# Kernel tuning notes

Measured on AMD Instinct MI355X. Metric: run time of the kernel, lower is better.

## Reference

```python
import jax, jax.numpy as jnp
import numpy as np

KERNEL_SIZE = 5
GROUP_SIZE = 1
SCALE = 2


def setup_inputs() -> dict:
    key = jax.random.key(0)
    k1, k2 = jax.random.split(key)
    N, C, H, W = 2, 256, 128, 128
    features = jax.random.normal(k1, (N, C, H, W), dtype=jnp.float32)
    masks = jax.random.uniform(
        k2, (N, KERNEL_SIZE * KERNEL_SIZE * GROUP_SIZE, H * SCALE, W * SCALE),
        dtype=jnp.float32)
    return {"features": features, "masks": masks}


def reference(features, masks):
    # CARAFE: content-aware reassembly upsampling.
    # out[n,c,i,j] = sum_{dy,dx} feat[n,c, i//s + dy - r, j//s + dx - r]
    #                * masks[n, g*K*K + dy*K + dx, i, j]
    K, G, s = KERNEL_SIZE, GROUP_SIZE, SCALE
    N, C, H, W = features.shape
    Cg = C // G
    K2 = K * K
    r = K // 2
    # zero-pad spatially and gather all K*K shifted views -> (N, C, K2, H, W)
    fp = jnp.pad(features, ((0, 0), (0, 0), (r, r), (r, r)))
    patches = jnp.stack(
        [fp[:, :, dy:dy + H, dx:dx + W] for dy in range(K) for dx in range(K)],
        axis=2)
    patches = patches.reshape(N, G, Cg, K2, H, W)
    # masks at output resolution; split each output pixel into (src_pixel, subpixel)
    m = masks.reshape(N, G, K2, H, s, W, s)
    # weighted reduce over the kernel window, broadcast over channels in group
    out = jnp.einsum('ngckhw,ngkhawb->ngchawb', patches, m)
    return out.reshape(N, C, H * s, W * s)
```

## Files before the change

### kernel.cpp

```cpp
#include <hip/hip_runtime.h>

#define KK 5
#define RR 2
#define N_ 2
#define C_ 256
#define H_ 128
#define W_ 128
#define H2 256
#define W2 256
#define TW 32
#define TH 8
#define CCHUNK 8
#define PHh 12
#define PWw 36
#define NPIX (PHh*PWw)
#define PLANE (NPIX*4)
#define HW (H_*W_)
#define HW2 (H2*W2)
#define DEPTH 4

__global__ __launch_bounds__(256) void carafe_kernel(
    const float* __restrict__ feat,
    const float* __restrict__ masks,
    float* __restrict__ out)
{
    __shared__ float patch[2 * PLANE];

    const int tid = threadIdx.x;
    const int tx = tid & 31;
    const int ty = tid >> 5;

    const int bid   = blockIdx.x;
    const int xcd   = bid & 7;
    const int s     = bid >> 3;
    const int chunk = s & 31;
    const int tn    = xcd * 16 + (s >> 5);
    const int tile  = tn & 63;
    const int n     = tn >> 6;
    const int bx    = tile & 3;
    const int by    = tile >> 2;
    const int c0    = chunk * CCHUNK;

    const int i0 = by * TH + ty;
    const int j0 = bx * TW + tx;
    const int gy0 = by * TH - RR;
    const int gx0 = bx * TW - RR;

    const float* fbase = feat + (size_t)(n * C_ + c0) * HW;
    #pragma unroll
    for (int r = 0; r < 4; ++r) {
        const int idx = tid + r * 256;
        if (idx < 2 * NPIX) {
            const int G  = idx >= NPIX;
            const int p  = idx - G * NPIX;
            const int py = p / PWw;
            const int px = p - py * PWw;
            const int gy = gy0 + py;
            const int gx = gx0 + px;
            float4 v = make_float4(0.f, 0.f, 0.f, 0.f);
            if ((unsigned)gy < (unsigned)H_ && (unsigned)gx < (unsigned)W_) {
                const float* fp = fbase + (4 * G) * HW + gy * W_ + gx;
                v.x = fp[0];
                v.y = fp[HW];
                v.z = fp[2 * HW];
                v.w = fp[3 * HW];
            }
            *reinterpret_cast<float4*>(&patch[G * PLANE + p * 4]) = v;
        }
    }

    const float* mb = masks + ((size_t)n * (KK * KK) * H2 + (size_t)(2 * i0)) * W2 + 2 * j0;
    float2 q0[DEPTH], q1[DEPTH];
    #pragma unroll
    for (int t = 0; t < DEPTH; ++t) {
        q0[t] = *reinterpret_cast<const float2*>(mb + (size_t)t * HW2);
        q1[t] = *reinterpret_cast<const float2*>(mb + (size_t)t * HW2 + W2);
    }
    __syncthreads();

    float acc[CCHUNK][2][2] = {};
    const int p0 = ty * PWw + tx;

    #pragma unroll
    for (int k = 0; k < KK * KK; ++k) {
        const float2 m0 = q0[k % DEPTH];
        const float2 m1 = q1[k % DEPTH];
        if (k + DEPTH < KK * KK) {
            q0[k % DEPTH] = *reinterpret_cast<const float2*>(mb + (size_t)(k + DEPTH) * HW2);
            q1[k % DEPTH] = *reinterpret_cast<const float2*>(mb + (size_t)(k + DEPTH) * HW2 + W2);
        }
        const int dy = k / KK;
        const int dx = k - KK * dy;
        const int P  = p0 + dy * PWw + dx;
        const float4 v0 = *reinterpret_cast<const float4*>(&patch[P * 4]);
        const float4 v1 = *reinterpret_cast<const float4*>(&patch[PLANE + P * 4]);

        acc[0][0][0] += v0.x * m0.x;  acc[0][0][1] += v0.x * m0.y;
        acc[0][1][0] += v0.x * m1.x;  acc[0][1][1] += v0.x * m1.y;
        acc[1][0][0] += v0.y * m0.x;  acc[1][0][1] += v0.y * m0.y;
        acc[1][1][0] += v0.y * m1.x;  acc[1][1][1] += v0.y * m1.y;
        acc[2][0][0] += v0.z * m0.x;  acc[2][0][1] += v0.z * m0.y;
        acc[2][1][0] += v0.z * m1.x;  acc[2][1][1] += v0.z * m1.y;
        acc[3][0][0] += v0.w * m0.x;  acc[3][0][1] += v0.w * m0.y;
        acc[3][1][0] += v0.w * m1.x;  acc[3][1][1] += v0.w * m1.y;
        acc[4][0][0] += v1.x * m0.x;  acc[4][0][1] += v1.x * m0.y;
        acc[4][1][0] += v1.x * m1.x;  acc[4][1][1] += v1.x * m1.y;
        acc[5][0][0] += v1.y * m0.x;  acc[5][0][1] += v1.y * m0.y;
        acc[5][1][0] += v1.y * m1.x;  acc[5][1][1] += v1.y * m1.y;
        acc[6][0][0] += v1.z * m0.x;  acc[6][0][1] += v1.z * m0.y;
        acc[6][1][0] += v1.z * m1.x;  acc[6][1][1] += v1.z * m1.y;
        acc[7][0][0] += v1.w * m0.x;  acc[7][0][1] += v1.w * m0.y;
        acc[7][1][0] += v1.w * m1.x;  acc[7][1][1] += v1.w * m1.y;
    }

    float* ob = out + ((size_t)(n * C_ + c0) * H2 + (size_t)(2 * i0)) * W2 + 2 * j0;
    #pragma unroll
    for (int c = 0; c < CCHUNK; ++c) {
        *reinterpret_cast<float2*>(ob)      = make_float2(acc[c][0][0], acc[c][0][1]);
        *reinterpret_cast<float2*>(ob + W2) = make_float2(acc[c][1][0], acc[c][1][1]);
        ob += (size_t)HW2;
    }
}

extern "C" void kernel_launch(void* const* d_in, const int* in_sizes, int n_in,
                              void* d_out, int out_size, void* d_ws, size_t ws_size,
                              hipStream_t stream) {
    const float* feat  = (const float*)d_in[0];
    const float* masks = (const float*)d_in[1];
    float* out = (float*)d_out;

    carafe_kernel<<<dim3(4096), dim3(256), 0, stream>>>(feat, masks, out);
}
```

Measured before the change: 49.00 us.

## Remap threads to two pixels by four channels with register sliding window

Each thread now covers two adjacent source columns and four channels, not one column and eight channels. Per kernel row it loads six float4 patch values from LDS into registers and reuses them across the five dx taps, which cuts LDS reads. The LDS row stride is padded to avoid bank conflicts. Mask loads and output stores become 16-byte wide, and outputs use nontemporal stores. Mask values are now loaded twice, once by each channel-group half of the block.

```diff
diff --git a/kernel.cpp b/kernel.cpp
--- a/kernel.cpp
+++ b/kernel.cpp
@@ -13,11 +13,14 @@
 #define CCHUNK 8
 #define PHh 12
 #define PWw 36
+#define PWST 37
 #define NPIX (PHh*PWw)
-#define PLANE (NPIX*4)
+#define PLANE (PHh*PWST*4)
 #define HW (H_*W_)
 #define HW2 (H2*W2)
 #define DEPTH 4
+
+typedef float f32x4 __attribute__((ext_vector_type(4)));
 
 __global__ __launch_bounds__(256) void carafe_kernel(
     const float* __restrict__ feat,
@@ -27,8 +30,10 @@
     __shared__ float patch[2 * PLANE];
 
     const int tid = threadIdx.x;
-    const int tx = tid & 31;
-    const int ty = tid >> 5;
+    const int G   = tid >> 7;
+    const int pp  = tid & 127;
+    const int u   = pp & 15;
+    const int ty  = pp >> 4;
 
     const int bid   = blockIdx.x;
     const int xcd   = bid & 7;
@@ -42,7 +47,7 @@
     const int c0    = chunk * CCHUNK;
 
     const int i0 = by * TH + ty;
-    const int j0 = bx * TW + tx;
+    const int j0 = bx * TW + 2 * u;
     const int gy0 = by * TH - RR;
     const int gx0 = bx * TW - RR;
 
@@ -51,73 +56,72 @@
     for (int r = 0; r < 4; ++r) {
         const int idx = tid + r * 256;
         if (idx < 2 * NPIX) {
-            const int G  = idx >= NPIX;
-            const int p  = idx - G * NPIX;
+            const int Gs = idx >= NPIX;
+            const int p  = idx - Gs * NPIX;
             const int py = p / PWw;
             const int px = p - py * PWw;
             const int gy = gy0 + py;
             const int gx = gx0 + px;
             float4 v = make_float4(0.f, 0.f, 0.f, 0.f);
             if ((unsigned)gy < (unsigned)H_ && (unsigned)gx < (unsigned)W_) {
-                const float* fp = fbase + (4 * G) * HW + gy * W_ + gx;
+                const float* fp = fbase + (4 * Gs) * HW + gy * W_ + gx;
                 v.x = fp[0];
                 v.y = fp[HW];
                 v.z = fp[2 * HW];
                 v.w = fp[3 * HW];
             }
-            *reinterpret_cast<float4*>(&patch[G * PLANE + p * 4]) = v;
+            *reinterpret_cast<float4*>(&patch[Gs * PLANE + (py * PWST + px) * 4]) = v;
         }
     }
 
     const float* mb = masks + ((size_t)n * (KK * KK) * H2 + (size_t)(2 * i0)) * W2 + 2 * j0;
-    float2 q0[DEPTH], q1[DEPTH];
+    float4 q0[DEPTH], q1[DEPTH];
     #pragma unroll
     for (int t = 0; t < DEPTH; ++t) {
-        q0[t] = *reinterpret_cast<const float2*>(mb + (size_t)t * HW2);
-        q1[t] = *reinterpret_cast<const float2*>(mb + (size_t)t * HW2 + W2);
+        q0[t] = *reinterpret_cast<const float4*>(mb + (size_t)t * HW2);
+        q1[t] = *reinterpret_cast<const float4*>(mb + (size_t)t * HW2 + W2);
     }
     __syncthreads();
 
-    float acc[CCHUNK][2][2] = {};
-    const int p0 = ty * PWw + tx;
+    float acc[4][2][4] = {};
+    const int rbase = G * PLANE;
 
     #pragma unroll
-    for (int k = 0; k < KK * KK; ++k) {
-        const float2 m0 = q0[k % DEPTH];
-        const float2 m1 = q1[k % DEPTH];
-        if (k + DEPTH < KK * KK) {
-            q0[k % DEPTH] = *reinterpret_cast<const float2*>(mb + (size_t)(k + DEPTH) * HW2);
-            q1[k % DEPTH] = *reinterpret_cast<const float2*>(mb + (size_t)(k + DEPTH) * HW2 + W2);
+    for (int dy = 0; dy < KK; ++dy) {
+        const int row = ty + dy;
+        float4 w[6];
+        #pragma unroll
+        for (int j = 0; j < 6; ++j)
+            w[j] = *reinterpret_cast<const float4*>(&patch[rbase + (row * PWST + 2 * u + j) * 4]);
+
+        #pragma unroll
+        for (int dx = 0; dx < KK; ++dx) {
+            const int k = dy * KK + dx;
+            const float4 m0 = q0[k % DEPTH];
+            const float4 m1 = q1[k % DEPTH];
+            if (k + DEPTH < KK * KK) {
+                q0[k % DEPTH] = *reinterpret_cast<const float4*>(mb + (size_t)(k + DEPTH) * HW2);
+                q1[k % DEPTH] = *reinterpret_cast<const float4*>(mb + (size_t)(k + DEPTH) * HW2 + W2);
+            }
+            const float w0[4] = { w[dx].x,     w[dx].y,     w[dx].z,     w[dx].w     };
+            const float w1[4] = { w[dx + 1].x, w[dx + 1].y, w[dx + 1].z, w[dx + 1].w };
+            #pragma unroll
+            for (int t = 0; t < 4; ++t) {
+                acc[t][0][0] += w0[t] * m0.x;  acc[t][0][1] += w0[t] * m0.y;
+                acc[t][0][2] += w1[t] * m0.z;  acc[t][0][3] += w1[t] * m0.w;
+                acc[t][1][0] += w0[t] * m1.x;  acc[t][1][1] += w0[t] * m1.y;
+                acc[t][1][2] += w1[t] * m1.z;  acc[t][1][3] += w1[t] * m1.w;
+            }
         }
-        const int dy = k / KK;
-        const int dx = k - KK * dy;
-        const int P  = p0 + dy * PWw + dx;
-        const float4 v0 = *reinterpret_cast<const float4*>(&patch[P * 4]);
-        const float4 v1 = *reinterpret_cast<const float4*>(&patch[PLANE + P * 4]);
-
-        acc[0][0][0] += v0.x * m0.x;  acc[0][0][1] += v0.x * m0.y;
-        acc[0][1][0] += v0.x * m1.x;  acc[0][1][1] += v0.x * m1.y;
-        acc[1][0][0] += v0.y * m0.x;  acc[1][0][1] += v0.y * m0.y;
-        acc[1][1][0] += v0.y * m1.x;  acc[1][1][1] += v0.y * m1.y;
-        acc[2][0][0] += v0.z * m0.x;  acc[2][0][1] += v0.z * m0.y;
-        acc[2][1][0] += v0.z * m1.x;  acc[2][1][1] += v0.z * m1.y;
-        acc[3][0][0] += v0.w * m0.x;  acc[3][0][1] += v0.w * m0.y;
-        acc[3][1][0] += v0.w * m1.x;  acc[3][1][1] += v0.w * m1.y;
-        acc[4][0][0] += v1.x * m0.x;  acc[4][0][1] += v1.x * m0.y;
-        acc[4][1][0] += v1.x * m1.x;  acc[4][1][1] += v1.x * m1.y;
-        acc[5][0][0] += v1.y * m0.x;  acc[5][0][1] += v1.y * m0.y;
-        acc[5][1][0] += v1.y * m1.x;  acc[5][1][1] += v1.y * m1.y;
-        acc[6][0][0] += v1.z * m0.x;  acc[6][0][1] += v1.z * m0.y;
-        acc[6][1][0] += v1.z * m1.x;  acc[6][1][1] += v1.z * m1.y;
-        acc[7][0][0] += v1.w * m0.x;  acc[7][0][1] += v1.w * m0.y;
-        acc[7][1][0] += v1.w * m1.x;  acc[7][1][1] += v1.w * m1.y;
     }
 
-    float* ob = out + ((size_t)(n * C_ + c0) * H2 + (size_t)(2 * i0)) * W2 + 2 * j0;
+    float* ob = out + ((size_t)(n * C_ + c0 + 4 * G) * H2 + (size_t)(2 * i0)) * W2 + 2 * j0;
     #pragma unroll
-    for (int c = 0; c < CCHUNK; ++c) {
-        *reinterpret_cast<float2*>(ob)      = make_float2(acc[c][0][0], acc[c][0][1]);
-        *reinterpret_cast<float2*>(ob + W2) = make_float2(acc[c][1][0], acc[c][1][1]);
+    for (int t = 0; t < 4; ++t) {
+        f32x4 r0; r0.x = acc[t][0][0]; r0.y = acc[t][0][1]; r0.z = acc[t][0][2]; r0.w = acc[t][0][3];
+        f32x4 r1; r1.x = acc[t][1][0]; r1.y = acc[t][1][1]; r1.z = acc[t][1][2]; r1.w = acc[t][1][3];
+        __builtin_nontemporal_store(r0, reinterpret_cast<f32x4*>(ob));
+        __builtin_nontemporal_store(r1, reinterpret_cast<f32x4*>(ob + W2));
         ob += (size_t)HW2;
     }
 }
```

New measurement: 51.90 us. 1.06x slower.
